# Performance work log

Measured on AMD Instinct MI355X. Metric: run time of the kernel, lower is better.

## Reference

```python
import jax, jax.numpy as jnp
import numpy as np

# FVM mesh / U-Net hierarchy sizes
NC = 1_000_000   # cell centers
NF = 1_500_000   # faces
N0 = 500_000     # points level 0
N1 = 125_000
N2 = 31_250
N3 = 7_813
N4 = 1_954
WSTD = 0.02      # weight scale keeps activations bounded through deep scatter-add stack


def _edges(key, e, n_src, n_dst):
    k1, k2 = jax.random.split(key)
    src = jax.random.randint(k1, (e,), 0, n_src)
    dst = jax.random.randint(k2, (e,), 0, n_dst)
    return jnp.stack([src, dst]).astype(jnp.int64)


def setup_inputs() -> dict:
    key = jax.random.key(0)
    ks = iter(jax.random.split(key, 64))
    inp = {}
    inp['xc'] = jax.random.normal(next(ks), (NC, 2), jnp.float32)
    inp['xf'] = jax.random.normal(next(ks), (NF, 4), jnp.float32)
    # bipartite relations
    edge_defs = [
        ('cf', 3_000_000, NC, NF), ('fp', 3_000_000, NF, N0), ('pc', 4_000_000, N0, NC),
        ('pp0', 3_500_000, N0, N0), ('pp1', 875_000, N1, N1), ('pp2', 218_750, N2, N2),
        ('pp3', 54_691, N3, N3), ('pp4', 13_678, N4, N4),
        ('pool0', 1_000_000, N0, N1), ('pool1', 250_000, N1, N2),
        ('pool2', 62_500, N2, N3), ('pool3', 15_626, N3, N4),
        ('unpool0', 1_000_000, N1, N0), ('unpool1', 250_000, N2, N1),
        ('unpool2', 62_500, N3, N2), ('unpool3', 15_626, N4, N3),
    ]
    for name, e, ns, nd in edge_defs:
        inp[name + '_ei'] = _edges(next(ks), e, ns, nd)
        inp[name + '_ea'] = jax.random.uniform(next(ks), (e,), jnp.float32)
    # learned parameters (edge-conditioned conv weights + biases)
    wdefs = [('W_cf', 2, 12), ('W_fp', 16, 16), ('W2', 16, 16), ('W3', 16, 16),
             ('W4', 16, 32), ('W5a', 32, 32), ('W5b', 32, 32), ('W6', 64, 32),
             ('W7', 48, 32), ('W8', 48, 16), ('W9a', 32, 16), ('W9b', 16, 16),
             ('Wf', 16, 1)]
    for name, fi, fo in wdefs:
        inp[name] = jax.random.normal(next(ks), (fi, fo), jnp.float32) * WSTD
        inp[name.replace('W', 'b', 1)] = jnp.zeros((fo,), jnp.float32)
    return inp


def gconv(x, ei, ea, W, b, n_out):
    """Edge-conditioned graph conv: gather src, linear, edge-weight, scatter-add, ReLU."""
    m = (x[ei[0]] @ W) * ea[:, None]                       # [E, out]
    return jax.nn.relu(jax.ops.segment_sum(m, ei[1], num_segments=n_out) + b)


def scatter_w(x, ei, ea, n_out):
    """Weighted scatter-add used by CustomPoolingAdd / CustomUnpooling."""
    return jax.ops.segment_sum(ea[:, None] * x[ei[0]], ei[1], num_segments=n_out)


def reference(xc, xf,
              cf_ei, cf_ea, fp_ei, fp_ea, pc_ei, pc_ea,
              pp0_ei, pp0_ea, pp1_ei, pp1_ea, pp2_ei, pp2_ea, pp3_ei, pp3_ea, pp4_ei, pp4_ea,
              pool0_ei, pool0_ea, pool1_ei, pool1_ea, pool2_ei, pool2_ea, pool3_ei, pool3_ea,
              unpool0_ei, unpool0_ea, unpool1_ei, unpool1_ea, unpool2_ei, unpool2_ea,
              unpool3_ei, unpool3_ea,
              W_cf, b_cf, W_fp, b_fp, W2, b2, W3, b3, W4, b4,
              W5a, b5a, W5b, b5b, W6, b6, W7, b7, W8, b8,
              W9a, b9a, W9b, b9b, Wf, bf):
    # _ConvBlock1: centers -> faces, concat face feats, faces -> points
    h = gconv(xc, cf_ei, cf_ea, W_cf, b_cf, NF)            # [NF,12]
    c1 = gconv(jnp.concatenate([h, xf], -1), fp_ei, fp_ea, W_fp, b_fp, N0)  # [N0,16]
    # encoder: pool then point-point conv
    c2 = gconv(scatter_w(c1, pool0_ei, pool0_ea, N1), pp1_ei, pp1_ea, W2, b2, N1)
    c3 = gconv(scatter_w(c2, pool1_ei, pool1_ea, N2), pp2_ei, pp2_ea, W3, b3, N2)
    c4 = gconv(scatter_w(c3, pool2_ei, pool2_ea, N3), pp3_ei, pp3_ea, W4, b4, N3)  # [N3,32]
    # bottleneck (_ConvBlock5): pool, 2 convs, unpool
    c5 = scatter_w(c4, pool3_ei, pool3_ea, N4)
    c5 = gconv(c5, pp4_ei, pp4_ea, W5a, b5a, N4)
    c5 = gconv(c5, pp4_ei, pp4_ea, W5b, b5b, N4)
    c5 = scatter_w(c5, unpool3_ei, unpool3_ea, N3)          # [N3,32]
    # decoder: skip-concat, conv, unpool
    c6 = scatter_w(gconv(jnp.concatenate([c5, c4], -1), pp3_ei, pp3_ea, W6, b6, N3),
                   unpool2_ei, unpool2_ea, N2)
    c7 = scatter_w(gconv(jnp.concatenate([c6, c3], -1), pp2_ei, pp2_ea, W7, b7, N2),
                   unpool1_ei, unpool1_ea, N1)
    c8 = scatter_w(gconv(jnp.concatenate([c7, c2], -1), pp1_ei, pp1_ea, W8, b8, N1),
                   unpool0_ei, unpool0_ea, N0)
    # _ConvBlock9: point-point conv then points -> cell centers
    c9 = gconv(jnp.concatenate([c8, c1], -1), pp0_ei, pp0_ea, W9a, b9a, N0)
    c9 = gconv(c9, pc_ei, pc_ea, W9b, b9b, NC)              # [NC,16]
    # _ConvBlock10 / SelfLoopLayer: per-node linear readout
    return c9 @ Wf + bf                                     # [NC,1]
```

## Files before the change

kernel.cpp:

```cpp
#include <hip/hip_runtime.h>
#include <cstdint>
#include <cstddef>


#define DEV __device__ __forceinline__

static constexpr int NCc = 1000000;
static constexpr int NFc = 1500000;
static constexpr int N0c = 500000;
static constexpr int N1c = 125000;
static constexpr int N2c = 31250;
static constexpr int N3c = 7813;
static constexpr int N4c = 1954;
static constexpr int SCHUNK = 8192;
static constexpr int CH = 16384;
static constexpr size_t ZDCAP = 17690000;

struct BuildTab {
    const int*   src[14];
    const int*   dst[14];
    const float* ea[14];
    int chunkBase[15];
    int binBase[15];
    int moff[14];
    int doff[14];
    int E[14];
    int nblk[14];
    int nbins[14];
    int nsets;
};


template<int NB>
__global__ void __launch_bounds__(1024)
mhist_k(BuildTab tab, int* __restrict__ histG)
{
    __shared__ int sh[NB];
    int j = blockIdx.x, t = 0;
    while (j >= tab.chunkBase[t + 1]) ++t;
    int lj = j - tab.chunkBase[t];
    int nbins = tab.nbins[t], nblk = tab.nblk[t], E = tab.E[t];
    const int* __restrict__ dst = tab.dst[t];
    int* hg = histG + tab.moff[t];
    int tx = threadIdx.x;
    for (int i = tx; i < nbins; i += 1024) sh[i] = 0;
    __syncthreads();
    int base = lj * CH + tx;
    for (int k0 = 0; k0 < 16; k0 += 8) {
        int d8[8];
#pragma unroll
        for (int k = 0; k < 8; ++k) {
            int e = base + (k0 + k) * 1024;
            d8[k] = (e < E) ? dst[e] : -1;
        }
#pragma unroll
        for (int k = 0; k < 8; ++k)
            if (d8[k] >= 0) atomicAdd(&sh[d8[k] >> 10], 1);
    }
    __syncthreads();
    for (int i = tx; i < nbins; i += 1024) hg[i * nblk + lj] = sh[i];
}

template<int NB>
__global__ void __launch_bounds__(1024)
mscat_k(BuildTab tab, const int* __restrict__ scanS, int2* __restrict__ brec)
{
    __shared__ int cnt[NB];
    __shared__ int bas[NB];
    int j = blockIdx.x, t = 0;
    while (j >= tab.chunkBase[t + 1]) ++t;
    int lj = j - tab.chunkBase[t];
    int nbins = tab.nbins[t], nblk = tab.nblk[t], E = tab.E[t];
    const int* __restrict__ src = tab.src[t];
    const int* __restrict__ dst = tab.dst[t];
    const float* __restrict__ ea = tab.ea[t];
    const int* sc = scanS + tab.moff[t];
    int tx = threadIdx.x;
    for (int i = tx; i < nbins; i += 1024) { cnt[i] = 0; bas[i] = sc[i * nblk + lj]; }
    __syncthreads();
    int base = lj * CH + tx;
    for (int k0 = 0; k0 < 16; k0 += 4) {
        int d4[4], s4[4]; float w4[4];
#pragma unroll
        for (int k = 0; k < 4; ++k) {
            int e = base + (k0 + k) * 1024;
            d4[k] = (e < E) ? dst[e] : -1;
            s4[k] = (e < E) ? src[e] : 0;
            w4[k] = (e < E) ? ea[e] : 0.f;
        }
#pragma unroll
        for (int k = 0; k < 4; ++k) {
            if (d4[k] >= 0) {
                int bl = d4[k] >> 10;
                int r = atomicAdd(&cnt[bl], 1);
                brec[bas[bl] + r] =
                    make_int2(((d4[k] & 1023) << 21) | s4[k], __float_as_int(w4[k]));
            }
        }
    }
}

__global__ void __launch_bounds__(1024)
mcsr_k(BuildTab tab, const int2* __restrict__ brec, const int* __restrict__ scanS,
       int* __restrict__ starts, int2* __restrict__ poolG, int sbias)
{
    __shared__ int cnt[1024];
    __shared__ int lst[1024];
    __shared__ int sd[1024];
    int b = blockIdx.x, t = 0;
    while (b >= tab.binBase[t + 1]) ++t;
    int bl = b - tab.binBase[t];
    int nblk = tab.nblk[t];
    int mo = tab.moff[t];
    int tx = threadIdx.x;
    int bs = scanS[mo + bl * nblk];
    int be = scanS[mo + (bl + 1) * nblk];
    cnt[tx] = 0;
    __syncthreads();
    int i = bs + tx;
    for (; i + 3072 < be; i += 4096) {
        int2 r0 = brec[i], r1 = brec[i + 1024], r2 = brec[i + 2048], r3 = brec[i + 3072];
        atomicAdd(&cnt[(unsigned)r0.x >> 21], 1);
        atomicAdd(&cnt[(unsigned)r1.x >> 21], 1);
        atomicAdd(&cnt[(unsigned)r2.x >> 21], 1);
        atomicAdd(&cnt[(unsigned)r3.x >> 21], 1);
    }
    for (; i < be; i += 1024) atomicAdd(&cnt[(unsigned)brec[i].x >> 21], 1);
    __syncthreads();
    int v = cnt[tx];
    sd[tx] = v; __syncthreads();
    for (int off = 1; off < 1024; off <<= 1) {
        int y = (tx >= off) ? sd[tx - off] : 0;
        __syncthreads();
        sd[tx] += y;
        __syncthreads();
    }
    lst[tx] = sd[tx] - v;
    __syncthreads();
    int* startsSet = starts + tab.doff[t];
    int gb = sbias + bs;
    startsSet[(bl << 10) + tx] = gb + lst[tx];
    cnt[tx] = 0;
    __syncthreads();
    i = bs + tx;
    for (; i < be; i += 1024) {
        int2 rec = brec[i];
        int dl = (unsigned)rec.x >> 21;
        int r = atomicAdd(&cnt[dl], 1);
        poolG[bs + lst[dl] + r] = make_int2(rec.x & 0x1FFFFF, rec.y);
    }
}

__global__ void __launch_bounds__(256)
scan1_k(const int* deg, int* starts, int* part, int n)
{
    __shared__ int sd[256];
    int t = threadIdx.x;
    int base = blockIdx.x * SCHUNK + t * 32;
    int v[32]; int sum = 0;
#pragma unroll
    for (int k = 0; k < 32; ++k) { int i = base + k; v[k] = (i < n) ? deg[i] : 0; sum += v[k]; }
    sd[t] = sum; __syncthreads();
    for (int off = 1; off < 256; off <<= 1) {
        int y = (t >= off) ? sd[t - off] : 0;
        __syncthreads();
        sd[t] += y;
        __syncthreads();
    }
    int run = sd[t] - sum;
#pragma unroll
    for (int k = 0; k < 32; ++k) { int i = base + k; if (i < n) starts[i] = run; run += v[k]; }
    if (t == 255) part[blockIdx.x] = sd[255];
}

__global__ void __launch_bounds__(1024)
scan2_k(int* __restrict__ part, int nb)
{
    __shared__ int sd[1024];
    int t = threadIdx.x;
    int v = (t < nb) ? part[t] : 0;
    sd[t] = v; __syncthreads();
    for (int off = 1; off < 1024; off <<= 1) {
        int y = (t >= off) ? sd[t - off] : 0;
        __syncthreads();
        sd[t] += y;
        __syncthreads();
    }
    if (t < nb) part[t] = sd[t] - v;
}

__global__ void __launch_bounds__(256)
scan3_k(int* __restrict__ starts, const int* __restrict__ part, int n, int Etot)
{
    int i = blockIdx.x * 256 + threadIdx.x;
    if (i < n) starts[i] += part[i / SCHUNK];
    if (i == 0) starts[n] = Etot;
}

template<int F>
DEV void row_fma(const float* __restrict__ p, float w, float* acc)
{
    static_assert(F % 4 == 0, "");
#pragma unroll
    for (int k = 0; k < F; k += 4) {
        float4 v = *reinterpret_cast<const float4*>(p + k);
        acc[k+0] = fmaf(w, v.x, acc[k+0]); acc[k+1] = fmaf(w, v.y, acc[k+1]);
        acc[k+2] = fmaf(w, v.z, acc[k+2]); acc[k+3] = fmaf(w, v.w, acc[k+3]);
    }
}

__global__ void __launch_bounds__(256)
cffp_k(const float* __restrict__ xc, const float* __restrict__ xf,
       const int2* __restrict__ ecsr, const int* __restrict__ starts,
       const float* __restrict__ W_cf, const float* __restrict__ b_cf,
       const float* __restrict__ W_fp, float* __restrict__ t, int n)
{
    __shared__ float sWcf[24];
    __shared__ float sbcf[12];
    __shared__ float sWfp[256];
    for (int i = threadIdx.x; i < 24;  i += 256) sWcf[i] = W_cf[i];
    for (int i = threadIdx.x; i < 12;  i += 256) sbcf[i] = b_cf[i];
    for (int i = threadIdx.x; i < 256; i += 256) sWfp[i] = W_fp[i];
    __syncthreads();
    int d = blockIdx.x * 256 + threadIdx.x;
    if (d >= n) return;
    int i0 = starts[d], i1 = starts[d + 1];
    float a0 = 0.f, a1 = 0.f;
    for (int i = i0; i < i1; ++i) {
        int2 rec = ecsr[i];
        float2 v = *reinterpret_cast<const float2*>(xc + (size_t)rec.x * 2);
        float w = __int_as_float(rec.y);
        a0 = fmaf(w, v.x, a0); a1 = fmaf(w, v.y, a1);
    }
    float h12[12];
#pragma unroll
    for (int j = 0; j < 12; ++j)
        h12[j] = fmaxf(fmaf(a0, sWcf[j], fmaf(a1, sWcf[12 + j], sbcf[j])), 0.f);
    float4 xfv = *reinterpret_cast<const float4*>(xf + (size_t)d * 4);
    float* op = t + (size_t)d * 16;
#pragma unroll
    for (int o = 0; o < 16; o += 4) {
        float4 y; float* yp = &y.x;
#pragma unroll
        for (int jj = 0; jj < 4; ++jj) {
            int oo = o + jj;
            float s =      xfv.x * sWfp[12 * 16 + oo];
            s = fmaf(xfv.y, sWfp[13 * 16 + oo], s);
            s = fmaf(xfv.z, sWfp[14 * 16 + oo], s);
            s = fmaf(xfv.w, sWfp[15 * 16 + oo], s);
#pragma unroll
            for (int j = 0; j < 12; ++j) s = fmaf(h12[j], sWfp[j * 16 + oo], s);
            yp[jj] = s;
        }
        *reinterpret_cast<float4*>(op + o) = y;
    }
}

template<int F, bool EPI>
__global__ void __launch_bounds__(256)
gather_sw_k(const float* __restrict__ x, const int2* __restrict__ ecsr,
            const int* __restrict__ starts, const float* __restrict__ b,
            float* __restrict__ out, int n)
{
    int d = blockIdx.x * 256 + threadIdx.x;
    if (d >= n) return;
    int i0 = starts[d], i1 = starts[d + 1];
    float acc[F];
#pragma unroll
    for (int k = 0; k < F; ++k) acc[k] = 0.f;
    for (int i = i0; i < i1; ++i) {
        int2 rec = ecsr[i];
        row_fma<F>(x + (size_t)rec.x * F, __int_as_float(rec.y), acc);
    }
    if constexpr (EPI) {
#pragma unroll
        for (int k = 0; k < F; ++k) acc[k] = fmaxf(acc[k] + b[k], 0.f);
    }
    float* op = out + (size_t)d * F;
#pragma unroll
    for (int k = 0; k < F; k += 4)
        *reinterpret_cast<float4*>(op + k) = make_float4(acc[k], acc[k+1], acc[k+2], acc[k+3]);
}

template<int FI1, int FI2, int FO>
__global__ void __launch_bounds__(256)
gather_conv_k(const float* __restrict__ x1, const float* __restrict__ x2,
              const int2* __restrict__ ecsr, const int* __restrict__ starts,
              const float* __restrict__ W, const float* __restrict__ b,
              float* __restrict__ out, int n)
{
    constexpr int FI = FI1 + FI2;
    __shared__ float sW[FI * FO];
    for (int i = threadIdx.x; i < FI * FO; i += 256) sW[i] = W[i];
    __syncthreads();
    int d = blockIdx.x * 256 + threadIdx.x;
    if (d >= n) return;
    int i0 = starts[d], i1 = starts[d + 1];
    float acc[FI];
#pragma unroll
    for (int k = 0; k < FI; ++k) acc[k] = 0.f;
    for (int i = i0; i < i1; ++i) {
        int2 rec = ecsr[i];
        float w = __int_as_float(rec.y);
        row_fma<FI1>(x1 + (size_t)rec.x * FI1, w, acc);
        if constexpr (FI2 > 0)
            row_fma<FI2>(x2 + (size_t)rec.x * FI2, w, acc + FI1);
    }
    float* op = out + (size_t)d * FO;
#pragma unroll
    for (int fo = 0; fo < FO; fo += 4) {
        float4 y; float* yp = &y.x;
#pragma unroll
        for (int j = 0; j < 4; ++j) {
            float s = b[fo + j];
#pragma unroll
            for (int k = 0; k < FI; ++k) s = fmaf(acc[k], sW[k * FO + fo + j], s);
            yp[j] = fmaxf(s, 0.f);
        }
        *reinterpret_cast<float4*>(op + fo) = y;
    }
}

template<int F1, int F2, int FO, bool EPIB>
__global__ void __launch_bounds__(256)
gather_dense_k(const float* __restrict__ x, const float* __restrict__ x2,
               const int2* __restrict__ ecsr, const int* __restrict__ starts,
               const float* __restrict__ bpre, const float* __restrict__ W,
               float* __restrict__ out, int n)
{
    constexpr int FI = F1 + F2;
    __shared__ float sW[FI * FO];
    for (int i = threadIdx.x; i < FI * FO; i += 256) sW[i] = W[i];
    __syncthreads();
    int d = blockIdx.x * 256 + threadIdx.x;
    if (d >= n) return;
    int i0 = starts[d], i1 = starts[d + 1];
    float acc[F1];
#pragma unroll
    for (int k = 0; k < F1; ++k) acc[k] = 0.f;
    for (int i = i0; i < i1; ++i) {
        int2 rec = ecsr[i];
        row_fma<F1>(x + (size_t)rec.x * F1, __int_as_float(rec.y), acc);
    }
    if constexpr (EPIB) {
#pragma unroll
        for (int k = 0; k < F1; ++k) acc[k] = fmaxf(acc[k] + bpre[k], 0.f);
    }
    float xin2[F2 > 0 ? F2 : 1];
    if constexpr (F2 > 0) {
        const float* p = x2 + (size_t)d * F2;
#pragma unroll
        for (int k = 0; k < F2; k += 4) {
            float4 v = *reinterpret_cast<const float4*>(p + k);
            xin2[k] = v.x; xin2[k+1] = v.y; xin2[k+2] = v.z; xin2[k+3] = v.w;
        }
    }
    float* op = out + (size_t)d * FO;
#pragma unroll
    for (int fo = 0; fo < FO; fo += 4) {
        float4 y; float* yp = &y.x;
#pragma unroll
        for (int j = 0; j < 4; ++j) {
            float s = 0.f;
#pragma unroll
            for (int k = 0; k < F1; ++k) s = fmaf(acc[k], sW[k * FO + fo + j], s);
            if constexpr (F2 > 0)
#pragma unroll
                for (int k = 0; k < F2; ++k) s = fmaf(xin2[k], sW[(F1 + k) * FO + fo + j], s);
            yp[j] = s;
        }
        *reinterpret_cast<float4*>(op + fo) = y;
    }
}

__global__ void __launch_bounds__(256)
gather_final_k(const float* __restrict__ x, const int2* __restrict__ ecsr,
               const int* __restrict__ starts, const float* __restrict__ b9b,
               const float* __restrict__ Wf, const float* __restrict__ bf,
               float* __restrict__ out, int n)
{
    int d = blockIdx.x * 256 + threadIdx.x;
    if (d >= n) return;
    int i0 = starts[d], i1 = starts[d + 1];
    float acc[16];
#pragma unroll
    for (int k = 0; k < 16; ++k) acc[k] = 0.f;
    for (int i = i0; i < i1; ++i) {
        int2 rec = ecsr[i];
        row_fma<16>(x + (size_t)rec.x * 16, __int_as_float(rec.y), acc);
    }
    float y = bf[0];
#pragma unroll
    for (int k = 0; k < 16; ++k) y = fmaf(fmaxf(acc[k] + b9b[k], 0.f), Wf[k], y);
    out[d] = y;
}

extern "C" void kernel_launch(void* const* d_in, const int* in_sizes, int n_in,
                              void* d_out, int out_size, void* d_ws, size_t ws_size,
                              hipStream_t stream)
{
    const float* xc = (const float*)d_in[0];
    const float* xf = (const float*)d_in[1];

    auto SRC = [&](int i) { return (const int*)d_in[i]; };
    auto DST = [&](int i) { return (const int*)d_in[i] + in_sizes[i] / 2; };
    auto EA  = [&](int i) { return (const float*)d_in[i + 1]; };
    auto EN  = [&](int i) { return in_sizes[i] / 2; };

    const float* W_cf=(const float*)d_in[34]; const float* b_cf=(const float*)d_in[35];
    const float* W_fp=(const float*)d_in[36]; const float* b_fp=(const float*)d_in[37];
    const float* W2  =(const float*)d_in[38]; const float* b2  =(const float*)d_in[39];
    const float* W3  =(const float*)d_in[40]; const float* b3  =(const float*)d_in[41];
    const float* W4  =(const float*)d_in[42]; const float* b4  =(const float*)d_in[43];
    const float* W5a =(const float*)d_in[44]; const float* b5a =(const float*)d_in[45];
    const float* W5b =(const float*)d_in[46]; const float* b5b =(const float*)d_in[47];
    const float* W6  =(const float*)d_in[48]; const float* b6  =(const float*)d_in[49];
    const float* W7  =(const float*)d_in[50]; const float* b7  =(const float*)d_in[51];
    const float* W8  =(const float*)d_in[52]; const float* b8  =(const float*)d_in[53];
    const float* W9a =(const float*)d_in[54]; const float* b9a =(const float*)d_in[55];
    const float* W9b =(const float*)d_in[56]; const float* b9b =(const float*)d_in[57];
    const float* Wf  =(const float*)d_in[58]; const float* bfb =(const float*)d_in[59];

    float* ws = (float*)d_ws;
    auto pad4 = [](size_t x) { return (x + 3) & ~(size_t)3; };
    auto nbinsOf = [](int nd) { return (nd + 1023) >> 10; };

    const int sI_in[2]  = {2, 4};
    const int sI_nd[2]  = {NFc, N0c};
    const int sII_in[14] = {6, 8, 10, 12, 14, 16, 18, 20, 22, 24, 26, 28, 30, 32};
    const int sII_nd[14] = {NCc, N0c, N1c, N2c, N3c, N4c, N1c, N2c, N3c, N4c,
                            N0c, N1c, N2c, N3c};

    size_t sumNdPadI = 0, sumEI = 0, sumNdPadII = 0, sumEII = 0;
    for (int t = 0; t < 2;  ++t) { sumNdPadI  += (size_t)nbinsOf(sI_nd[t])  << 10; sumEI  += EN(sI_in[t]); }
    for (int t = 0; t < 14; ++t) { sumNdPadII += (size_t)nbinsOf(sII_nd[t]) << 10; sumEII += EN(sII_in[t]); }
    size_t zI  = pad4(sumNdPadI  + 1) + pad4(2 * sumEI);
    size_t zII = pad4(sumNdPadII + 1) + pad4(2 * sumEII);
    size_t zAB = (zI > zII) ? zI : zII;
    size_t zD_o   = zAB;
    size_t part_o = zD_o + ZDCAP;
    size_t zC_o   = part_o + 1024;
    size_t t_o    = zI;

    int* part = (int*)(ws + part_o);
    const int B = 256;
    auto G = [&](int n) { return dim3((unsigned)((n + B - 1) / B)); };

    auto buildStage = [&](int ns, const int* sin, const int* snd,
                          int* starts, int2* pool, int* doffOut) {
        int nbinsA[14], nblkA[14];
        long long eoffA[14];
        long long sumNdPad = 0, sumE = 0;
        for (int t = 0; t < ns; ++t) {
            int nd = snd[t], E = EN(sin[t]);
            doffOut[t] = (int)sumNdPad;
            nbinsA[t] = (nd + 1023) >> 10;
            sumNdPad += (long long)nbinsA[t] << 10;
            nblkA[t] = (E + CH - 1) / CH;
            eoffA[t] = sumE;
            sumE += E;
        }
        int t0 = 0;
        while (t0 < ns) {
            long long cost = 0; int t1 = t0;
            while (t1 < ns) {
                long long c = 2LL * EN(sin[t1]) + (long long)nbinsA[t1] * nblkA[t1];
                if (t1 > t0 && cost + c + 1 > (long long)ZDCAP) break;
                cost += c; ++t1;
            }
            BuildTab tb{};
            int gn = t1 - t0, tc = 0, tbn = 0, maxNb = 0;
            long long LA = 0, gE = 0;
            for (int t = t0; t < t1; ++t) {
                int q = t - t0;
                tb.src[q] = SRC(sin[t]); tb.dst[q] = DST(sin[t]); tb.ea[q] = EA(sin[t]);
                tb.chunkBase[q] = tc; tb.binBase[q] = tbn;
                tb.moff[q] = (int)LA; tb.doff[q] = doffOut[t];
                tb.E[q] = EN(sin[t]); tb.nblk[q] = nblkA[t]; tb.nbins[q] = nbinsA[t];
                tc += nblkA[t]; tbn += nbinsA[t];
                LA += (long long)nbinsA[t] * nblkA[t]; gE += EN(sin[t]);
                if (nbinsA[t] > maxNb) maxNb = nbinsA[t];
            }
            tb.chunkBase[gn] = tc; tb.binBase[gn] = tbn; tb.nsets = gn;
            int2* brec = (int2*)(ws + zD_o);
            int*  hist = (int*)(ws + zD_o) + 2 * gE;
            if (maxNb > 1024)
                mhist_k<2048><<<dim3((unsigned)tc), 1024, 0, stream>>>(tb, hist);
            else
                mhist_k<1024><<<dim3((unsigned)tc), 1024, 0, stream>>>(tb, hist);
            int nb = (int)((LA + SCHUNK - 1) / SCHUNK);
            scan1_k<<<dim3((unsigned)nb), B, 0, stream>>>(hist, hist, part, (int)LA);
            scan2_k<<<dim3(1), 1024, 0, stream>>>(part, nb);
            scan3_k<<<G((int)LA + 1), B, 0, stream>>>(hist, part, (int)LA, (int)gE);
            if (maxNb > 1024)
                mscat_k<2048><<<dim3((unsigned)tc), 1024, 0, stream>>>(tb, hist, brec);
            else
                mscat_k<1024><<<dim3((unsigned)tc), 1024, 0, stream>>>(tb, hist, brec);
            long long gBase = eoffA[t0];
            mcsr_k<<<dim3((unsigned)tbn), 1024, 0, stream>>>(
                tb, brec, hist, starts, pool + gBase, (int)gBase);
            t0 = t1;
        }
    };

    float* t   = ws + t_o;
    float* c1  = ws + zC_o;
    float* tpc = c1;
    size_t mb = zD_o;
    auto mal = [&](size_t n) { size_t o = mb; mb += pad4(n); return ws + o; };
    float* p1  = mal((size_t)N1c*16);
    float* c2  = mal((size_t)N1c*16);
    float* p2  = mal((size_t)N2c*16);
    float* c3  = mal((size_t)N2c*16);
    float* p3  = mal((size_t)N3c*16);
    float* c4  = mal((size_t)N3c*32);
    float* p4  = mal((size_t)N4c*32);
    float* c5a = mal((size_t)N4c*32);
    float* c5b = mal((size_t)N4c*32);
    float* t6  = mal((size_t)N3c*32);
    float* g6  = mal((size_t)N3c*32);
    float* t7  = mal((size_t)N2c*32);
    float* g7  = mal((size_t)N2c*32);
    float* t8  = mal((size_t)N1c*16);
    float* g8  = mal((size_t)N1c*16);
    float* t9  = ws + zD_o;
    float* out = (float*)d_out;

    int* startsI = (int*)(ws + 0);
    int2* poolI  = (int2*)(ws + pad4(sumNdPadI + 1));
    int doffI[2];
    buildStage(2, sI_in, sI_nd, startsI, poolI, doffI);
    cffp_k<<<G(NFc), B, 0, stream>>>(
        xc, xf, poolI, startsI + doffI[0], W_cf, b_cf, W_fp, t, NFc);
    gather_sw_k<16,true><<<G(N0c), B, 0, stream>>>(
        t, poolI, startsI + doffI[1], b_fp, c1, N0c);

    int* startsII = (int*)(ws + 0);
    int2* poolII  = (int2*)(ws + pad4(sumNdPadII + 1));
    int doffII[14];
    buildStage(14, sII_in, sII_nd, startsII, poolII, doffII);
    enum { f_pc, f_pp0, f_pp1, f_pp2, f_pp3, f_pp4, f_po0, f_po1, f_po2, f_po3,
           f_up0, f_up1, f_up2, f_up3 };
    auto st = [&](int t_) { return startsII + doffII[t_]; };
    int2* ec = poolII;

    gather_sw_k<16,false><<<G(N1c), B, 0, stream>>>(c1, ec, st(f_po0), nullptr, p1, N1c);
    gather_conv_k<16,0,16><<<G(N1c), B, 0, stream>>>(p1, nullptr, ec, st(f_pp1), W2, b2, c2, N1c);
    gather_sw_k<16,false><<<G(N2c), B, 0, stream>>>(c2, ec, st(f_po1), nullptr, p2, N2c);
    gather_conv_k<16,0,16><<<G(N2c), B, 0, stream>>>(p2, nullptr, ec, st(f_pp2), W3, b3, c3, N2c);
    gather_sw_k<16,false><<<G(N3c), B, 0, stream>>>(c3, ec, st(f_po2), nullptr, p3, N3c);
    gather_conv_k<16,0,32><<<G(N3c), B, 0, stream>>>(p3, nullptr, ec, st(f_pp3), W4, b4, c4, N3c);
    gather_sw_k<32,false><<<G(N4c), B, 0, stream>>>(c4, ec, st(f_po3), nullptr, p4, N4c);
    gather_conv_k<32,0,32><<<G(N4c), B, 0, stream>>>(p4, nullptr, ec, st(f_pp4), W5a, b5a, c5a, N4c);
    gather_conv_k<32,0,32><<<G(N4c), B, 0, stream>>>(c5a, nullptr, ec, st(f_pp4), W5b, b5b, c5b, N4c);
    gather_dense_k<32,32,32,false><<<G(N3c), B, 0, stream>>>(
        c5b, c4, ec, st(f_up3), nullptr, W6, t6, N3c);
    gather_sw_k<32,true><<<G(N3c), B, 0, stream>>>(t6, ec, st(f_pp3), b6, g6, N3c);
    gather_dense_k<32,16,32,false><<<G(N2c), B, 0, stream>>>(
        g6, c3, ec, st(f_up2), nullptr, W7, t7, N2c);
    gather_sw_k<32,true><<<G(N2c), B, 0, stream>>>(t7, ec, st(f_pp2), b7, g7, N2c);
    gather_dense_k<32,16,16,false><<<G(N1c), B, 0, stream>>>(
        g7, c2, ec, st(f_up1), nullptr, W8, t8, N1c);
    gather_sw_k<16,true><<<G(N1c), B, 0, stream>>>(t8, ec, st(f_pp1), b8, g8, N1c);
    gather_dense_k<16,16,16,false><<<G(N0c), B, 0, stream>>>(
        g8, c1, ec, st(f_up0), nullptr, W9a, t9, N0c);
    gather_dense_k<16,0,16,true><<<G(N0c), B, 0, stream>>>(
        t9, nullptr, ec, st(f_pp0), b9a, W9b, tpc, N0c);
    gather_final_k<<<G(NCc), B, 0, stream>>>(tpc, ec, st(f_pc), b9b, Wf, bfb, out, NCc);
}
```

Baseline: 1.513 ms.

## Stage bucket-scatter records in shared memory for coalesced global writes

The bucket scatter kernel now processes each chunk in two halves. Each half builds a local histogram, prefix-scans it and groups the records by bucket in LDS, then writes them out contiguously per bucket. Previously every record went straight to a scattered global address. The goal is more coalesced writes, paid for with more shared memory (lower occupancy), many barriers and a serial 1024-wide scan per half.

```diff
diff --git a/kernel.cpp b/kernel.cpp
--- a/kernel.cpp
+++ b/kernel.cpp
@@ -14,6 +14,7 @@
 static constexpr int N4c = 1954;
 static constexpr int SCHUNK = 8192;
 static constexpr int CH = 16384;
+static constexpr int HALF = 8192;
 static constexpr size_t ZDCAP = 17690000;
 
 struct BuildTab {
@@ -45,7 +46,7 @@
     int tx = threadIdx.x;
     for (int i = tx; i < nbins; i += 1024) sh[i] = 0;
     __syncthreads();
-    int base = lj * CH + tx;
+    int base = j == j ? lj * CH + tx : 0;
     for (int k0 = 0; k0 < 16; k0 += 8) {
         int d8[8];
 #pragma unroll
@@ -65,8 +66,13 @@
 __global__ void __launch_bounds__(1024)
 mscat_k(BuildTab tab, const int* __restrict__ scanS, int2* __restrict__ brec)
 {
-    __shared__ int cnt[NB];
+    __shared__ int hcnt[NB];
     __shared__ int bas[NB];
+    __shared__ int cum[NB];
+    __shared__ int lstart[NB];
+    __shared__ int sd[1024];
+    __shared__ int2 srec[HALF];
+    __shared__ unsigned short sbkt[HALF];
     int j = blockIdx.x, t = 0;
     while (j >= tab.chunkBase[t + 1]) ++t;
     int lj = j - tab.chunkBase[t];
@@ -76,27 +82,68 @@
     const float* __restrict__ ea = tab.ea[t];
     const int* sc = scanS + tab.moff[t];
     int tx = threadIdx.x;
-    for (int i = tx; i < nbins; i += 1024) { cnt[i] = 0; bas[i] = sc[i * nblk + lj]; }
-    __syncthreads();
-    int base = lj * CH + tx;
-    for (int k0 = 0; k0 < 16; k0 += 4) {
-        int d4[4], s4[4]; float w4[4];
-#pragma unroll
-        for (int k = 0; k < 4; ++k) {
-            int e = base + (k0 + k) * 1024;
-            d4[k] = (e < E) ? dst[e] : -1;
-            s4[k] = (e < E) ? src[e] : 0;
-            w4[k] = (e < E) ? ea[e] : 0.f;
-        }
-#pragma unroll
-        for (int k = 0; k < 4; ++k) {
-            if (d4[k] >= 0) {
-                int bl = d4[k] >> 10;
-                int r = atomicAdd(&cnt[bl], 1);
-                brec[bas[bl] + r] =
-                    make_int2(((d4[k] & 1023) << 21) | s4[k], __float_as_int(w4[k]));
+    for (int i = tx; i < NB; i += 1024) cum[i] = 0;
+    for (int i = tx; i < nbins; i += 1024) bas[i] = sc[i * nblk + lj];
+    __syncthreads();
+
+    for (int h = 0; h < CH / HALF; ++h) {
+        for (int i = tx; i < NB; i += 1024) hcnt[i] = 0;
+        __syncthreads();
+        int bl8[8], r8[8]; int2 rec8[8];
+        int base = lj * CH + h * HALF + tx;
+#pragma unroll
+        for (int k = 0; k < 8; ++k) {
+            int e = base + k * 1024;
+            if (e < E) {
+                int d = dst[e];
+                bl8[k] = d >> 10;
+                rec8[k] = make_int2(((d & 1023) << 21) | src[e],
+                                    __float_as_int(ea[e]));
+                r8[k] = atomicAdd(&hcnt[bl8[k]], 1);
+            } else bl8[k] = -1;
+        }
+        __syncthreads();
+        if constexpr (NB == 1024) {
+            int v = hcnt[tx];
+            sd[tx] = v; __syncthreads();
+            for (int off = 1; off < 1024; off <<= 1) {
+                int y = (tx >= off) ? sd[tx - off] : 0;
+                __syncthreads();
+                sd[tx] += y;
+                __syncthreads();
             }
-        }
+            lstart[tx] = sd[tx] - v;
+        } else {
+            int v0 = hcnt[tx * 2], v1 = hcnt[tx * 2 + 1];
+            int s = v0 + v1;
+            sd[tx] = s; __syncthreads();
+            for (int off = 1; off < 1024; off <<= 1) {
+                int y = (tx >= off) ? sd[tx - off] : 0;
+                __syncthreads();
+                sd[tx] += y;
+                __syncthreads();
+            }
+            int run = sd[tx] - s;
+            lstart[tx * 2] = run; lstart[tx * 2 + 1] = run + v0;
+        }
+        __syncthreads();
+        int tot = lstart[NB - 1] + hcnt[NB - 1];
+#pragma unroll
+        for (int k = 0; k < 8; ++k) {
+            if (bl8[k] >= 0) {
+                int pos = lstart[bl8[k]] + r8[k];
+                srec[pos] = rec8[k];
+                sbkt[pos] = (unsigned short)bl8[k];
+            }
+        }
+        __syncthreads();
+        for (int pos = tx; pos < tot; pos += 1024) {
+            int b = sbkt[pos];
+            brec[bas[b] + cum[b] + (pos - lstart[b])] = srec[pos];
+        }
+        __syncthreads();
+        for (int i = tx; i < NB; i += 1024) cum[i] += hcnt[i];
+        __syncthreads();
     }
 }
 
```

After: 1.362 ms. 1.11x faster.
